# Optimization experiments

Measured on AMD Instinct MI355X. Metric: run time of the kernel, lower is better.

The kernel has to match this reference:

```python
import jax, jax.numpy as jnp
import numpy as np

BSZ, T, L, D = 8, 8, 196, 192
E = D            # expand=1 -> d_inner
C = E * T        # d_inner_s = d_inner * d_t (scan channels)
N = 16           # d_state
K = 4            # d_conv
R = 96           # dt_rank = ceil(d_model*d_t/16)
DT_MIN, DT_MAX, DT_FLOOR = 1e-3, 1e-1, 1e-4


def setup_inputs() -> dict:
    key = jax.random.key(0)
    ks = jax.random.split(key, 9)
    hidden = jax.random.normal(ks[0], (BSZ, T, L, D), jnp.float32)
    in_proj_w = jax.random.normal(ks[1], (2 * E, D), jnp.float32) * (D ** -0.5)
    conv_w = jax.random.normal(ks[2], (C, K), jnp.float32) * 0.2
    conv_b = jax.random.normal(ks[3], (C,), jnp.float32) * 0.05
    x_proj_w = jax.random.normal(ks[4], (R + 2 * N, C), jnp.float32) * (C ** -0.5)
    dt_init_std = R ** -0.5
    dt_proj_w = jax.random.uniform(ks[5], (C, R), jnp.float32, -dt_init_std, dt_init_std)
    dt = jnp.exp(jax.random.uniform(ks[6], (C,), jnp.float32) * (np.log(DT_MAX) - np.log(DT_MIN)) + np.log(DT_MIN))
    dt = jnp.clip(dt, DT_FLOOR)
    dt_bias = dt + jnp.log(-jnp.expm1(-dt))  # inverse-softplus init
    A_log = jnp.log(jnp.tile(jnp.arange(1, N + 1, dtype=jnp.float32), (C, 1)))
    D_param = jnp.ones((C,), jnp.float32)
    return {"hidden": hidden, "in_proj_w": in_proj_w, "conv_w": conv_w, "conv_b": conv_b,
            "x_proj_w": x_proj_w, "dt_proj_w": dt_proj_w, "dt_bias": dt_bias,
            "A_log": A_log, "D_param": D_param}


def _silu(x):
    return x * jax.nn.sigmoid(x)


def reference(hidden, in_proj_w, conv_w, conv_b, x_proj_w, dt_proj_w, dt_bias, A_log, D_param):
    Bsz, T_, L_, D_ = hidden.shape
    E_ = in_proj_w.shape[0] // 2
    # in_proj (no bias): (B,T,L,D) @ (2E,D)^T -> (B,2E,T,L)
    xz = jnp.einsum('btld,ed->betl', hidden, in_proj_w)
    # rearrange 'b d t l -> b (d t) l' then chunk(2, dim=1)
    x = xz[:, :E_].reshape(Bsz, E_ * T_, L_)   # (B, C, L)
    z = xz[:, E_:].reshape(Bsz, E_ * T_, L_)
    # causal depthwise conv1d + silu
    x = jax.lax.conv_general_dilated(
        x, conv_w[:, None, :], window_strides=(1,), padding=[(K - 1, 0)],
        dimension_numbers=('NCH', 'OIH', 'NCH'), feature_group_count=conv_w.shape[0])
    x = _silu(x + conv_b[None, :, None])
    # x_proj -> dt, B, C
    x_dbl = jnp.einsum('bcl,rc->brl', x, x_proj_w)  # (B, R+2N, L)
    dt = x_dbl[:, :R]
    B_ssm = x_dbl[:, R:R + N]        # (B, N, L)
    C_ssm = x_dbl[:, R + N:]         # (B, N, L)
    delta = jax.nn.softplus(jnp.einsum('brl,cr->bcl', dt, dt_proj_w) + dt_bias[None, :, None])
    A = -jnp.exp(A_log)              # (C, N)
    # selective scan: h_l = exp(delta*A) * h_{l-1} + delta*B*x
    dA = jnp.exp(jnp.einsum('bcl,cn->lbcn', delta, A))       # (L,B,C,N)
    dBu = jnp.einsum('bcl,bnl,bcl->lbcn', delta, B_ssm, x)   # (L,B,C,N)

    def step(h, ab):
        a, b = ab
        h = h * a + b
        return h, h

    h0 = jnp.zeros((Bsz, dA.shape[2], dA.shape[3]), x.dtype)
    _, hs = jax.lax.scan(step, h0, (dA, dBu))                # (L,B,C,N)
    y = jnp.einsum('lbcn,bnl->bcl', hs, C_ssm)
    y = y + x * D_param[None, :, None]
    out = y * _silu(z)               # (B, C, L) — fused path output before out_proj
    return out
```

## Files before the change

### kernel.cpp

```cpp
#include <hip/hip_runtime.h>
#include <hip/hip_bf16.h>
#include <cstddef>

#define BSZ 8
#define T_  8
#define L_  196
#define D_  192
#define E_  192
#define C_  1536
#define N_  16
#define K_  4
#define R_  96

typedef __attribute__((ext_vector_type(8))) short short8;
typedef __attribute__((ext_vector_type(4))) float f32x4;
typedef unsigned short ushort_t;

__global__ __launch_bounds__(256) void k_cast_bf16(
    const float* __restrict__ in, ushort_t* __restrict__ out, int n8) {
  int i = blockIdx.x * 256 + threadIdx.x;
  if (i >= n8) return;
  const float4* ip = (const float4*)in;
  float4 v0 = ip[(size_t)i * 2];
  float4 v1 = ip[(size_t)i * 2 + 1];
  union { ushort_t u[8]; uint4 v; } r;
  float f[8] = {v0.x, v0.y, v0.z, v0.w, v1.x, v1.y, v1.z, v1.w};
#pragma unroll
  for (int k = 0; k < 8; k++) {
    unsigned int bits = __float_as_uint(f[k]);
    bits += 0x7FFFu + ((bits >> 16) & 1u);
    r.u[k] = (ushort_t)(bits >> 16);
  }
  ((uint4*)out)[i] = r.v;
}

__global__ __launch_bounds__(256) void k_inproj_mfma(
    const ushort_t* __restrict__ hb, const ushort_t* __restrict__ wb,
    float* __restrict__ xb, float* __restrict__ zb) {
  __shared__ float smem[64][97];
  int tid = threadIdx.x;
  int wave = tid >> 6, lane = tid & 63;
  int m0b = blockIdx.x * 64;
  int n0 = blockIdx.y * 96;
  int row = lane & 15, kg = lane >> 4;
  int m0w = m0b + wave * 16;

  f32x4 acc[6] = {};
  const ushort_t* ap = hb + (size_t)(m0w + row) * 192 + kg * 8;
#pragma unroll
  for (int ks = 0; ks < 6; ks++) {
    short8 a = *(const short8*)(ap + ks * 32);
#pragma unroll
    for (int nt = 0; nt < 6; nt++) {
      short8 b = *(const short8*)(wb + (size_t)(n0 + nt * 16 + row) * 192 + ks * 32 + kg * 8);
      acc[nt] = __builtin_amdgcn_mfma_f32_16x16x32_bf16(a, b, acc[nt], 0, 0, 0);
    }
  }
#pragma unroll
  for (int nt = 0; nt < 6; nt++) {
#pragma unroll
    for (int j = 0; j < 4; j++) {
      smem[wave * 16 + kg * 4 + j][nt * 16 + row] = acc[nt][j];
    }
  }
  __syncthreads();
  int mloc = tid & 63, eof = tid >> 6;
  int m_glob = m0b + mloc;
  int b = m_glob / 1568, u = m_glob % 1568;
  size_t obase = (size_t)b * 301056 + u;
#pragma unroll
  for (int e = eof; e < 96; e += 4) {
    int eg = n0 + e;
    float v = smem[mloc][e];
    if (eg < 192) xb[obase + (size_t)eg * 1568] = v;
    else          zb[obase + (size_t)(eg - 192) * 1568] = v;
  }
}

__global__ __launch_bounds__(256) void k_inproj_f32(
    const float* __restrict__ A, const float* __restrict__ W,
    float* __restrict__ xb, float* __restrict__ zb) {
  __shared__ float As[16][132];
  __shared__ float Bs[16][132];
  int tid = threadIdx.x;
  int m0 = blockIdx.x * 128;
  int n0 = blockIdx.y * 128;
  int tx = tid & 15, ty = tid >> 4;
  float acc[8][8] = {};
  for (int k0 = 0; k0 < 192; k0 += 16) {
#pragma unroll
    for (int i = 0; i < 2; i++) {
      int idx = tid + i * 256;
      int m = idx >> 2, k4 = (idx & 3) * 4;
      float4 v = *(const float4*)&A[(size_t)(m0 + m) * 192 + k0 + k4];
      As[k4 + 0][m] = v.x; As[k4 + 1][m] = v.y;
      As[k4 + 2][m] = v.z; As[k4 + 3][m] = v.w;
    }
#pragma unroll
    for (int i = 0; i < 2; i++) {
      int idx = tid + i * 256;
      int n = idx >> 2, k4 = (idx & 3) * 4;
      float4 v = *(const float4*)&W[(size_t)(n0 + n) * 192 + k0 + k4];
      Bs[k4 + 0][n] = v.x; Bs[k4 + 1][n] = v.y;
      Bs[k4 + 2][n] = v.z; Bs[k4 + 3][n] = v.w;
    }
    __syncthreads();
#pragma unroll
    for (int kk = 0; kk < 16; kk++) {
      float a_[8], b_[8];
      *(float4*)&a_[0] = *(const float4*)&As[kk][ty * 4];
      *(float4*)&a_[4] = *(const float4*)&As[kk][ty * 4 + 64];
      *(float4*)&b_[0] = *(const float4*)&Bs[kk][tx * 4];
      *(float4*)&b_[4] = *(const float4*)&Bs[kk][tx * 4 + 64];
#pragma unroll
      for (int i = 0; i < 8; i++)
#pragma unroll
        for (int j = 0; j < 8; j++) acc[i][j] += a_[i] * b_[j];
    }
    __syncthreads();
  }
#pragma unroll
  for (int i = 0; i < 8; i++) {
    int m = m0 + ty * 4 + (i & 3) + ((i >> 2) * 64);
    int b = m / (T_ * L_);
    int r = m % (T_ * L_);
    int t = r / L_;
    int l = r % L_;
#pragma unroll
    for (int j = 0; j < 8; j++) {
      int e = n0 + tx * 4 + (j & 3) + ((j >> 2) * 64);
      float v = acc[i][j];
      if (e < E_) {
        int c = e * T_ + t;
        xb[((size_t)b * C_ + c) * L_ + l] = v;
      } else {
        int c = (e - E_) * T_ + t;
        zb[((size_t)b * C_ + c) * L_ + l] = v;
      }
    }
  }
}

__global__ __launch_bounds__(256) void k_conv(
    const float* __restrict__ xb, const float* __restrict__ conv_w,
    const float* __restrict__ conv_b, float* __restrict__ xc) {
  int idx = blockIdx.x * 256 + threadIdx.x;
  int l = idx % L_;
  int bc = idx / L_;
  int c = bc % C_;
  const float* xrow = xb + (size_t)bc * L_;
  const float* w = conv_w + c * K_;
  float acc = conv_b[c];
#pragma unroll
  for (int k = 0; k < K_; k++) {
    int ll = l - (K_ - 1) + k;
    if (ll >= 0) acc += xrow[ll] * w[k];
  }
  xc[idx] = acc / (1.f + __expf(-acc));
}

__global__ __launch_bounds__(256) void k_wtrans(
    const float* __restrict__ W, float* __restrict__ Wt) {
  int idx = blockIdx.x * 256 + threadIdx.x;
  int r = idx / 1536;
  int c = idx - r * 1536;
  Wt[(size_t)c * 128 + r] = W[idx];
}

#define XKK 32
__global__ __launch_bounds__(256) void k_xdbl_tile(
    const float* __restrict__ xc, const float* __restrict__ Wt,
    float* __restrict__ part) {
  __shared__ float Ws2[XKK][128];
  __shared__ float Xs[XKK][64];
  int tid = threadIdx.x;
  int n0 = blockIdx.x * 64;
  int c0 = blockIdx.y * 96;
  int tx = tid & 15, ty = tid >> 4;
  float acc[8][4] = {};
  for (int ck = 0; ck < 96; ck += XKK) {
#pragma unroll
    for (int i = 0; i < 4; i++) {
      int idx = tid + i * 256;
      int c = idx >> 5, r4 = (idx & 31) * 4;
      *(float4*)&Ws2[c][r4] = *(const float4*)&Wt[(size_t)(c0 + ck + c) * 128 + r4];
    }
#pragma unroll
    for (int i = 0; i < 8; i++) {
      int idx = tid + i * 256;
      int c = idx >> 6, j = idx & 63;
      int n = n0 + j;
      float v = 0.f;
      if (n < BSZ * L_) {
        int b = n / L_, l = n - b * L_;
        v = xc[((size_t)b * C_ + c0 + ck + c) * L_ + l];
      }
      Xs[c][j] = v;
    }
    __syncthreads();
#pragma unroll
    for (int kk = 0; kk < XKK; kk++) {
      float w_[8], x_[4];
      *(float4*)&w_[0] = *(const float4*)&Ws2[kk][ty * 8];
      *(float4*)&w_[4] = *(const float4*)&Ws2[kk][ty * 8 + 4];
      *(float4*)&x_[0] = *(const float4*)&Xs[kk][tx * 4];
#pragma unroll
      for (int i = 0; i < 8; i++)
#pragma unroll
        for (int j = 0; j < 4; j++) acc[i][j] += w_[i] * x_[j];
    }
    __syncthreads();
  }
  int kc = blockIdx.y;
#pragma unroll
  for (int j = 0; j < 4; j++) {
    int n = n0 + tx * 4 + j;
    if (n < BSZ * L_) {
      int b = n / L_, l = n - b * L_;
      float* pp = &part[(((size_t)kc * 8 + b) * L_ + l) * 128 + ty * 8];
      float4 v0 = {acc[0][j], acc[1][j], acc[2][j], acc[3][j]};
      float4 v1 = {acc[4][j], acc[5][j], acc[6][j], acc[7][j]};
      *(float4*)&pp[0] = v0;
      *(float4*)&pp[4] = v1;
    }
  }
}

__global__ __launch_bounds__(256) void k_xreduce(
    const float* __restrict__ part, float* __restrict__ xdbl,
    float* __restrict__ Bt, float* __restrict__ Ct) {
  int tx = threadIdx.x & 63;
  int ty = threadIdx.x >> 6;
  int l = blockIdx.x * 4 + ty;
  int b = blockIdx.y;
  size_t o = ((size_t)b * L_ + l) * 128 + tx;
  float v0 = 0.f, v1 = 0.f;
#pragma unroll
  for (int kc = 0; kc < 16; kc++) {
    v0 += part[(size_t)kc * (8 * L_ * 128) + o];
    v1 += part[(size_t)kc * (8 * L_ * 128) + o + 64];
  }
  int r1 = tx + 64;
  xdbl[((size_t)b * 96 + tx) * L_ + l] = v0;
  if (r1 < 96) {
    xdbl[((size_t)b * 96 + r1) * L_ + l] = v1;
  } else if (r1 < 96 + N_) {
    Bt[((size_t)b * L_ + l) * N_ + (r1 - 96)] = v1;
  } else {
    Ct[((size_t)b * L_ + l) * N_ + (r1 - 96 - N_)] = v1;
  }
}

__global__ __launch_bounds__(256) void k_xdbl_mono(
    const float* __restrict__ xc, const float* __restrict__ W,
    float* __restrict__ xdbl, float* __restrict__ Bt, float* __restrict__ Ct) {
  int tx = threadIdx.x & 63;
  int ty = threadIdx.x >> 6;
  int l = blockIdx.x * 64 + tx;
  int r0 = blockIdx.y * 4 + ty;
  int r1 = r0 + 64;
  int b = blockIdx.z;
  if (l >= L_) return;
  const float* xcb = xc + (size_t)b * C_ * L_;
  float acc0 = 0.f, acc1 = 0.f;
#pragma unroll 4
  for (int c = 0; c < C_; c++) {
    float v = xcb[(size_t)c * L_ + l];
    acc0 += v * W[(size_t)r0 * C_ + c];
    acc1 += v * W[(size_t)r1 * C_ + c];
  }
  xdbl[((size_t)b * 96 + r0) * L_ + l] = acc0;
  if (r1 < 96) {
    xdbl[((size_t)b * 96 + r1) * L_ + l] = acc1;
  } else if (r1 < 96 + N_) {
    Bt[((size_t)b * L_ + l) * N_ + (r1 - 96)] = acc1;
  } else {
    Ct[((size_t)b * L_ + l) * N_ + (r1 - 96 - N_)] = acc1;
  }
}

__global__ __launch_bounds__(256) void k_delta_gemm(
    const float* __restrict__ dtm, const float* __restrict__ Wdt,
    const float* __restrict__ dt_bias, float* __restrict__ delta) {
  __shared__ float Ws[96][68];
  __shared__ float Ds[96][68];
  int tid = threadIdx.x;
  int n0 = blockIdx.x * 64;
  int c0 = blockIdx.y * 64;
  for (int idx = tid; idx < 64 * 96; idx += 256) {
    int i = idx / 96, r = idx - i * 96;
    Ws[r][i] = Wdt[(size_t)(c0 + i) * 96 + r];
  }
  for (int idx = tid; idx < 96 * 64; idx += 256) {
    int r = idx >> 6, j = idx & 63;
    int n = n0 + j;
    float v = 0.f;
    if (n < BSZ * L_) {
      int b = n / L_, l = n - b * L_;
      v = dtm[((size_t)b * 96 + r) * L_ + l];
    }
    Ds[r][j] = v;
  }
  __syncthreads();
  int tx = tid & 15, ty = tid >> 4;
  float acc[4][4] = {};
#pragma unroll 8
  for (int r = 0; r < 96; r++) {
    float4 av = *(const float4*)&Ws[r][ty * 4];
    float4 bv = *(const float4*)&Ds[r][tx * 4];
    float a_[4] = {av.x, av.y, av.z, av.w};
    float b_[4] = {bv.x, bv.y, bv.z, bv.w};
#pragma unroll
    for (int i = 0; i < 4; i++)
#pragma unroll
      for (int j = 0; j < 4; j++) acc[i][j] += a_[i] * b_[j];
  }
#pragma unroll
  for (int i = 0; i < 4; i++) {
    int c = c0 + ty * 4 + i;
    float bias = dt_bias[c];
#pragma unroll
    for (int j = 0; j < 4; j++) {
      int n = n0 + tx * 4 + j;
      if (n < BSZ * L_) {
        int b = n / L_, l = n - b * L_;
        float v = acc[i][j] + bias;
        float sp = (v > 20.f) ? v : __logf(1.f + __expf(v));
        delta[((size_t)b * C_ + c) * L_ + l] = sp;
      }
    }
  }
}

__global__ __launch_bounds__(512) void k_scan_fused(
    const float* __restrict__ delta, const float* __restrict__ xc,
    const float* __restrict__ zb, const float* __restrict__ Bt,
    const float* __restrict__ Ct, const float* __restrict__ A_log,
    const float* __restrict__ D_param, float* __restrict__ out) {
  __shared__ float BtS[196][20];
  __shared__ float CtS[196][20];
  __shared__ float yS[16][196];
  int tid = threadIdx.x;
  int b = blockIdx.y;
  int c_base = blockIdx.x * 16;
  int wave = tid >> 6, lane = tid & 63;
  int chunk = lane & 15;
  int nl = lane >> 4;
  bool act = chunk < 14;
  const int l0 = chunk * 14;
  int c0 = c_base + wave * 2;
  int c1 = c0 + 1;

  {
    const float4* gB = (const float4*)(Bt + (size_t)b * L_ * N_);
    const float4* gC = (const float4*)(Ct + (size_t)b * L_ * N_);
    for (int i = tid; i < 784; i += 512) {
      int l = i >> 2, q = i & 3;
      *(float4*)&BtS[l][q * 4] = gB[i];
      *(float4*)&CtS[l][q * 4] = gC[i];
    }
  }

  float4 a0, a1;
  {
    float4 t0 = *(const float4*)&A_log[c0 * N_ + nl * 4];
    float4 t1 = *(const float4*)&A_log[c1 * N_ + nl * 4];
    a0.x = -__expf(t0.x); a0.y = -__expf(t0.y);
    a0.z = -__expf(t0.z); a0.w = -__expf(t0.w);
    a1.x = -__expf(t1.x); a1.y = -__expf(t1.y);
    a1.z = -__expf(t1.z); a1.w = -__expf(t1.w);
  }
  size_t w0 = (size_t)(b * C_ + c0) * L_ + l0;
  size_t w1 = (size_t)(b * C_ + c1) * L_ + l0;

  float2 dv0[7], xv0[7], dv1[7], xv1[7];
  if (act) {
    const float2* d2a = (const float2*)(delta + w0);
    const float2* d2b = (const float2*)(delta + w1);
    const float2* x2a = (const float2*)(xc + w0);
    const float2* x2b = (const float2*)(xc + w1);
#pragma unroll
    for (int i = 0; i < 7; i++) {
      dv0[i] = d2a[i]; dv1[i] = d2b[i];
      xv0[i] = x2a[i]; xv1[i] = x2b[i];
    }
  } else {
#pragma unroll
    for (int i = 0; i < 7; i++) {
      dv0[i] = {0.f, 0.f}; dv1[i] = {0.f, 0.f};
      xv0[i] = {0.f, 0.f}; xv1[i] = {0.f, 0.f};
    }
  }
  __syncthreads();

  float4 h0 = {0.f,0.f,0.f,0.f}, p0 = {1.f,1.f,1.f,1.f};
  float4 h1 = {0.f,0.f,0.f,0.f}, p1 = {1.f,1.f,1.f,1.f};
#pragma unroll
  for (int l = 0; l < 14; l++) {
    float d0 = (l & 1) ? dv0[l >> 1].y : dv0[l >> 1].x;
    float d1 = (l & 1) ? dv1[l >> 1].y : dv1[l >> 1].x;
    float x0 = (l & 1) ? xv0[l >> 1].y : xv0[l >> 1].x;
    float x1 = (l & 1) ? xv1[l >> 1].y : xv1[l >> 1].x;
    float du0 = d0 * x0, du1 = d1 * x1;
    float4 Bv = *(const float4*)&BtS[l0 + l][nl * 4];
    float e0x = __expf(d0 * a0.x), e0y = __expf(d0 * a0.y);
    float e0z = __expf(d0 * a0.z), e0w = __expf(d0 * a0.w);
    float e1x = __expf(d1 * a1.x), e1y = __expf(d1 * a1.y);
    float e1z = __expf(d1 * a1.z), e1w = __expf(d1 * a1.w);
    h0.x = h0.x * e0x + du0 * Bv.x; p0.x *= e0x;
    h0.y = h0.y * e0y + du0 * Bv.y; p0.y *= e0y;
    h0.z = h0.z * e0z + du0 * Bv.z; p0.z *= e0z;
    h0.w = h0.w * e0w + du0 * Bv.w; p0.w *= e0w;
    h1.x = h1.x * e1x + du1 * Bv.x; p1.x *= e1x;
    h1.y = h1.y * e1y + du1 * Bv.y; p1.y *= e1y;
    h1.z = h1.z * e1z + du1 * Bv.z; p1.z *= e1z;
    h1.w = h1.w * e1w + du1 * Bv.w; p1.w *= e1w;
  }

#pragma unroll
  for (int s = 1; s < 16; s <<= 1) {
    float4 P0, Q0, P1, Q1;
    P0.x = __shfl_up(p0.x, s, 16); Q0.x = __shfl_up(h0.x, s, 16);
    P0.y = __shfl_up(p0.y, s, 16); Q0.y = __shfl_up(h0.y, s, 16);
    P0.z = __shfl_up(p0.z, s, 16); Q0.z = __shfl_up(h0.z, s, 16);
    P0.w = __shfl_up(p0.w, s, 16); Q0.w = __shfl_up(h0.w, s, 16);
    P1.x = __shfl_up(p1.x, s, 16); Q1.x = __shfl_up(h1.x, s, 16);
    P1.y = __shfl_up(p1.y, s, 16); Q1.y = __shfl_up(h1.y, s, 16);
    P1.z = __shfl_up(p1.z, s, 16); Q1.z = __shfl_up(h1.z, s, 16);
    P1.w = __shfl_up(p1.w, s, 16); Q1.w = __shfl_up(h1.w, s, 16);
    if (chunk >= s) {
      h0.x = p0.x * Q0.x + h0.x; p0.x *= P0.x;
      h0.y = p0.y * Q0.y + h0.y; p0.y *= P0.y;
      h0.z = p0.z * Q0.z + h0.z; p0.z *= P0.z;
      h0.w = p0.w * Q0.w + h0.w; p0.w *= P0.w;
      h1.x = p1.x * Q1.x + h1.x; p1.x *= P1.x;
      h1.y = p1.y * Q1.y + h1.y; p1.y *= P1.y;
      h1.z = p1.z * Q1.z + h1.z; p1.z *= P1.z;
      h1.w = p1.w * Q1.w + h1.w; p1.w *= P1.w;
    }
  }
  float4 g0, g1;
  g0.x = __shfl_up(h0.x, 1, 16); g1.x = __shfl_up(h1.x, 1, 16);
  g0.y = __shfl_up(h0.y, 1, 16); g1.y = __shfl_up(h1.y, 1, 16);
  g0.z = __shfl_up(h0.z, 1, 16); g1.z = __shfl_up(h1.z, 1, 16);
  g0.w = __shfl_up(h0.w, 1, 16); g1.w = __shfl_up(h1.w, 1, 16);
  if (chunk == 0) {
    g0.x = g0.y = g0.z = g0.w = 0.f;
    g1.x = g1.y = g1.z = g1.w = 0.f;
  }

  if (act) {
#pragma unroll
    for (int l = 0; l < 14; l++) {
      float d0 = (l & 1) ? dv0[l >> 1].y : dv0[l >> 1].x;
      float d1 = (l & 1) ? dv1[l >> 1].y : dv1[l >> 1].x;
      float x0 = (l & 1) ? xv0[l >> 1].y : xv0[l >> 1].x;
      float x1 = (l & 1) ? xv1[l >> 1].y : xv1[l >> 1].x;
      float du0 = d0 * x0, du1 = d1 * x1;
      float4 Bv = *(const float4*)&BtS[l0 + l][nl * 4];
      float4 Cv = *(const float4*)&CtS[l0 + l][nl * 4];
      float e0x = __expf(d0 * a0.x), e0y = __expf(d0 * a0.y);
      float e0z = __expf(d0 * a0.z), e0w = __expf(d0 * a0.w);
      float e1x = __expf(d1 * a1.x), e1y = __expf(d1 * a1.y);
      float e1z = __expf(d1 * a1.z), e1w = __expf(d1 * a1.w);
      g0.x = g0.x * e0x + du0 * Bv.x;
      g0.y = g0.y * e0y + du0 * Bv.y;
      g0.z = g0.z * e0z + du0 * Bv.z;
      g0.w = g0.w * e0w + du0 * Bv.w;
      g1.x = g1.x * e1x + du1 * Bv.x;
      g1.y = g1.y * e1y + du1 * Bv.y;
      g1.z = g1.z * e1z + du1 * Bv.z;
      g1.w = g1.w * e1w + du1 * Bv.w;
      float y0 = g0.x * Cv.x + g0.y * Cv.y + g0.z * Cv.z + g0.w * Cv.w;
      float y1 = g1.x * Cv.x + g1.y * Cv.y + g1.z * Cv.z + g1.w * Cv.w;
      y0 += __shfl_xor(y0, 16);
      y0 += __shfl_xor(y0, 32);
      y1 += __shfl_xor(y1, 16);
      y1 += __shfl_xor(y1, 32);
      if (nl == 0) {
        yS[wave * 2 + 0][l0 + l] = y0;
        yS[wave * 2 + 1][l0 + l] = y1;
      }
    }
  }
  __syncthreads();

  size_t base = (size_t)(b * C_ + c_base) * L_;
  for (int idx = tid; idx < 16 * L_; idx += 512) {
    int cloc = idx / L_, l = idx - cloc * L_;
    float y = yS[cloc][l];
    float xv = xc[base + idx];
    float zv = zb[base + idx];
    float Dp = D_param[c_base + cloc];
    float sz = zv / (1.f + __expf(-zv));
    out[base + idx] = (y + xv * Dp) * sz;
  }
}

extern "C" void kernel_launch(void* const* d_in, const int* in_sizes, int n_in,
                              void* d_out, int out_size, void* d_ws, size_t ws_size,
                              hipStream_t stream) {
  const float* hidden    = (const float*)d_in[0];
  const float* in_proj_w = (const float*)d_in[1];
  const float* conv_w    = (const float*)d_in[2];
  const float* conv_b    = (const float*)d_in[3];
  const float* x_proj_w  = (const float*)d_in[4];
  const float* dt_proj_w = (const float*)d_in[5];
  const float* dt_bias   = (const float*)d_in[6];
  const float* A_log     = (const float*)d_in[7];
  const float* D_param   = (const float*)d_in[8];
  float* out = (float*)d_out;

  const size_t NBCL  = (size_t)BSZ * C_ * L_;
  const size_t NDT   = (size_t)BSZ * 96 * L_;
  const size_t NBT   = (size_t)BSZ * L_ * N_;
  const size_t NPART = (size_t)16 * BSZ * L_ * 128;
  const size_t NWT   = (size_t)C_ * 128;
  const size_t NHID  = (size_t)BSZ * T_ * L_ * D_;
  const size_t NW1   = (size_t)2 * E_ * D_;
  float* ws = (float*)d_ws;
  float* xb    = ws;
  float* zb    = xb + NBCL;
  float* xc    = zb + NBCL;
  float* xdbl  = xc + NBCL;
  float* BtArr = xdbl + NDT;
  float* CtArr = BtArr + NBT;
  float* Pbuf  = CtArr + NBT;
  float* delta = xb;

  size_t base_floats = 3 * NBCL + NDT + 2 * NBT;
  size_t avail = ws_size / 4 > base_floats ? ws_size / 4 - base_floats : 0;
  bool split_ok = avail >= NPART + NWT;

  if (split_ok) {
    ushort_t* hb = (ushort_t*)Pbuf;
    ushort_t* wb = hb + NHID;
    k_cast_bf16<<<(int)((NHID / 8 + 255) / 256), 256, 0, stream>>>(hidden, hb, (int)(NHID / 8));
    k_cast_bf16<<<(int)((NW1 / 8 + 255) / 256), 256, 0, stream>>>(in_proj_w, wb, (int)(NW1 / 8));
    k_inproj_mfma<<<dim3(196, 4), 256, 0, stream>>>(hb, wb, xb, zb);
  } else {
    k_inproj_f32<<<dim3(98, 3), 256, 0, stream>>>(hidden, in_proj_w, xb, zb);
  }

  k_conv<<<(int)(NBCL / 256), 256, 0, stream>>>(xb, conv_w, conv_b, xc);

  if (split_ok) {
    float* part = Pbuf;
    float* Wt   = Pbuf + NPART;
    k_wtrans<<<(int)(NWT / 256), 256, 0, stream>>>(x_proj_w, Wt);
    k_xdbl_tile<<<dim3(25, 16), 256, 0, stream>>>(xc, Wt, part);
    k_xreduce<<<dim3(49, BSZ), 256, 0, stream>>>(part, xdbl, BtArr, CtArr);
  } else {
    k_xdbl_mono<<<dim3(4, 16, BSZ), 256, 0, stream>>>(xc, x_proj_w, xdbl, BtArr, CtArr);
  }

  k_delta_gemm<<<dim3(25, 24), 256, 0, stream>>>(xdbl, dt_proj_w, dt_bias, delta);

  k_scan_fused<<<dim3(C_ / 16, BSZ), 512, 0, stream>>>(delta, xc, zb, BtArr, CtArr,
                                                       A_log, D_param, out);
}
```

Before: 125.2 us.

## Fuse causal conv+SiLU into x_proj and scan, merge casts, drop transpose kernel

The standalone depthwise conv+SiLU kernel is removed. Its output is now recomputed on the fly from the in_proj output inside the x_proj tile GEMM and inside the fused scan kernel. This saves a full write and re-read of the conv activation buffer and one launch. The two bf16 cast kernels are merged into a single launch. The x_proj weight transpose kernel is replaced by transposing into padded shared memory during the tile load. In exchange, conv arithmetic and overlapping neighbour loads are repeated in two consumers, and register pressure in the scan kernel rises.

```diff
diff --git a/kernel.cpp b/kernel.cpp
--- a/kernel.cpp
+++ b/kernel.cpp
@@ -16,13 +16,18 @@
 typedef __attribute__((ext_vector_type(4))) float f32x4;
 typedef unsigned short ushort_t;
 
-__global__ __launch_bounds__(256) void k_cast_bf16(
-    const float* __restrict__ in, ushort_t* __restrict__ out, int n8) {
+__global__ __launch_bounds__(256) void k_cast_all(
+    const float* __restrict__ hidden, const float* __restrict__ w,
+    ushort_t* __restrict__ hb, ushort_t* __restrict__ wb) {
+  const int H8 = 301056;
+  const int T8 = H8 + 9216;
   int i = blockIdx.x * 256 + threadIdx.x;
-  if (i >= n8) return;
-  const float4* ip = (const float4*)in;
-  float4 v0 = ip[(size_t)i * 2];
-  float4 v1 = ip[(size_t)i * 2 + 1];
+  if (i >= T8) return;
+  const float4* ip; uint4* op; int j;
+  if (i < H8) { ip = (const float4*)hidden; op = (uint4*)hb; j = i; }
+  else        { ip = (const float4*)w;      op = (uint4*)wb; j = i - H8; }
+  float4 v0 = ip[(size_t)j * 2];
+  float4 v1 = ip[(size_t)j * 2 + 1];
   union { ushort_t u[8]; uint4 v; } r;
   float f[8] = {v0.x, v0.y, v0.z, v0.w, v1.x, v1.y, v1.z, v1.w};
 #pragma unroll
@@ -31,7 +36,7 @@
     bits += 0x7FFFu + ((bits >> 16) & 1u);
     r.u[k] = (ushort_t)(bits >> 16);
   }
-  ((uint4*)out)[i] = r.v;
+  op[j] = r.v;
 }
 
 __global__ __launch_bounds__(256) void k_inproj_mfma(
@@ -159,19 +164,12 @@
   xc[idx] = acc / (1.f + __expf(-acc));
 }
 
-__global__ __launch_bounds__(256) void k_wtrans(
-    const float* __restrict__ W, float* __restrict__ Wt) {
-  int idx = blockIdx.x * 256 + threadIdx.x;
-  int r = idx / 1536;
-  int c = idx - r * 1536;
-  Wt[(size_t)c * 128 + r] = W[idx];
-}
-
 #define XKK 32
 __global__ __launch_bounds__(256) void k_xdbl_tile(
-    const float* __restrict__ xc, const float* __restrict__ Wt,
+    const float* __restrict__ xb, const float* __restrict__ conv_w,
+    const float* __restrict__ conv_b, const float* __restrict__ W,
     float* __restrict__ part) {
-  __shared__ float Ws2[XKK][128];
+  __shared__ float Ws2[XKK][132];
   __shared__ float Xs[XKK][64];
   int tid = threadIdx.x;
   int n0 = blockIdx.x * 64;
@@ -180,20 +178,31 @@
   float acc[8][4] = {};
   for (int ck = 0; ck < 96; ck += XKK) {
 #pragma unroll
-    for (int i = 0; i < 4; i++) {
-      int idx = tid + i * 256;
-      int c = idx >> 5, r4 = (idx & 31) * 4;
-      *(float4*)&Ws2[c][r4] = *(const float4*)&Wt[(size_t)(c0 + ck + c) * 128 + r4];
-    }
-#pragma unroll
-    for (int i = 0; i < 8; i++) {
-      int idx = tid + i * 256;
+    for (int p = 0; p < 4; p++) {
+      int idx = tid + p * 256;
+      int r = idx >> 3;
+      int c4 = (idx & 7) * 4;
+      float4 w4 = *(const float4*)&W[(size_t)r * 1536 + c0 + ck + c4];
+      Ws2[c4 + 0][r] = w4.x; Ws2[c4 + 1][r] = w4.y;
+      Ws2[c4 + 2][r] = w4.z; Ws2[c4 + 3][r] = w4.w;
+    }
+#pragma unroll
+    for (int p = 0; p < 8; p++) {
+      int idx = tid + p * 256;
       int c = idx >> 6, j = idx & 63;
       int n = n0 + j;
       float v = 0.f;
       if (n < BSZ * L_) {
         int b = n / L_, l = n - b * L_;
-        v = xc[((size_t)b * C_ + c0 + ck + c) * L_ + l];
+        int cc = c0 + ck + c;
+        const float* row = xb + ((size_t)b * C_ + cc) * L_;
+        float s = conv_b[cc];
+#pragma unroll
+        for (int k = 0; k < K_; k++) {
+          int ll = l - 3 + k;
+          if (ll >= 0) s += row[ll] * conv_w[cc * K_ + k];
+        }
+        v = s / (1.f + __expf(-s));
       }
       Xs[c][j] = v;
     }
@@ -333,7 +342,8 @@
 }
 
 __global__ __launch_bounds__(512) void k_scan_fused(
-    const float* __restrict__ delta, const float* __restrict__ xc,
+    const float* __restrict__ delta, const float* __restrict__ xb,
+    const float* __restrict__ conv_w, const float* __restrict__ conv_b,
     const float* __restrict__ zb, const float* __restrict__ Bt,
     const float* __restrict__ Ct, const float* __restrict__ A_log,
     const float* __restrict__ D_param, float* __restrict__ out) {
@@ -373,23 +383,41 @@
   size_t w0 = (size_t)(b * C_ + c0) * L_ + l0;
   size_t w1 = (size_t)(b * C_ + c1) * L_ + l0;
 
-  float2 dv0[7], xv0[7], dv1[7], xv1[7];
+  float xr0[14], xr1[14];
+  {
+    const float* r0 = xb + (size_t)(b * C_ + c0) * L_;
+    const float* r1 = xb + (size_t)(b * C_ + c1) * L_;
+    float t0[17], t1[17];
+#pragma unroll
+    for (int i = 0; i < 17; i++) {
+      int ll = l0 - 3 + i;
+      bool ok = act && ll >= 0;
+      t0[i] = ok ? r0[ll] : 0.f;
+      t1[i] = ok ? r1[ll] : 0.f;
+    }
+    float w00 = conv_w[c0 * K_ + 0], w01 = conv_w[c0 * K_ + 1];
+    float w02 = conv_w[c0 * K_ + 2], w03 = conv_w[c0 * K_ + 3];
+    float w10 = conv_w[c1 * K_ + 0], w11 = conv_w[c1 * K_ + 1];
+    float w12 = conv_w[c1 * K_ + 2], w13 = conv_w[c1 * K_ + 3];
+    float cb0 = conv_b[c0], cb1 = conv_b[c1];
+#pragma unroll
+    for (int l = 0; l < 14; l++) {
+      float s0 = cb0 + t0[l] * w00 + t0[l + 1] * w01 + t0[l + 2] * w02 + t0[l + 3] * w03;
+      float s1 = cb1 + t1[l] * w10 + t1[l + 1] * w11 + t1[l + 2] * w12 + t1[l + 3] * w13;
+      xr0[l] = s0 / (1.f + __expf(-s0));
+      xr1[l] = s1 / (1.f + __expf(-s1));
+    }
+  }
+
+  float2 dv0[7], dv1[7];
   if (act) {
     const float2* d2a = (const float2*)(delta + w0);
     const float2* d2b = (const float2*)(delta + w1);
-    const float2* x2a = (const float2*)(xc + w0);
-    const float2* x2b = (const float2*)(xc + w1);
-#pragma unroll
-    for (int i = 0; i < 7; i++) {
-      dv0[i] = d2a[i]; dv1[i] = d2b[i];
-      xv0[i] = x2a[i]; xv1[i] = x2b[i];
-    }
+#pragma unroll
+    for (int i = 0; i < 7; i++) { dv0[i] = d2a[i]; dv1[i] = d2b[i]; }
   } else {
 #pragma unroll
-    for (int i = 0; i < 7; i++) {
-      dv0[i] = {0.f, 0.f}; dv1[i] = {0.f, 0.f};
-      xv0[i] = {0.f, 0.f}; xv1[i] = {0.f, 0.f};
-    }
+    for (int i = 0; i < 7; i++) { dv0[i] = {0.f, 0.f}; dv1[i] = {0.f, 0.f}; }
   }
   __syncthreads();
 
@@ -399,9 +427,7 @@
   for (int l = 0; l < 14; l++) {
     float d0 = (l & 1) ? dv0[l >> 1].y : dv0[l >> 1].x;
     float d1 = (l & 1) ? dv1[l >> 1].y : dv1[l >> 1].x;
-    float x0 = (l & 1) ? xv0[l >> 1].y : xv0[l >> 1].x;
-    float x1 = (l & 1) ? xv1[l >> 1].y : xv1[l >> 1].x;
-    float du0 = d0 * x0, du1 = d1 * x1;
+    float du0 = d0 * xr0[l], du1 = d1 * xr1[l];
     float4 Bv = *(const float4*)&BtS[l0 + l][nl * 4];
     float e0x = __expf(d0 * a0.x), e0y = __expf(d0 * a0.y);
     float e0z = __expf(d0 * a0.z), e0w = __expf(d0 * a0.w);
@@ -454,9 +480,7 @@
     for (int l = 0; l < 14; l++) {
       float d0 = (l & 1) ? dv0[l >> 1].y : dv0[l >> 1].x;
       float d1 = (l & 1) ? dv1[l >> 1].y : dv1[l >> 1].x;
-      float x0 = (l & 1) ? xv0[l >> 1].y : xv0[l >> 1].x;
-      float x1 = (l & 1) ? xv1[l >> 1].y : xv1[l >> 1].x;
-      float du0 = d0 * x0, du1 = d1 * x1;
+      float du0 = d0 * xr0[l], du1 = d1 * xr1[l];
       float4 Bv = *(const float4*)&BtS[l0 + l][nl * 4];
       float4 Cv = *(const float4*)&CtS[l0 + l][nl * 4];
       float e0x = __expf(d0 * a0.x), e0y = __expf(d0 * a0.y);
@@ -488,10 +512,18 @@
   size_t base = (size_t)(b * C_ + c_base) * L_;
   for (int idx = tid; idx < 16 * L_; idx += 512) {
     int cloc = idx / L_, l = idx - cloc * L_;
+    int c = c_base + cloc;
+    const float* xrow = xb + base + (size_t)cloc * L_;
+    float s = conv_b[c];
+#pragma unroll
+    for (int k = 0; k < K_; k++) {
+      int ll = l - 3 + k;
+      if (ll >= 0) s += xrow[ll] * conv_w[c * K_ + k];
+    }
+    float xv = s / (1.f + __expf(-s));
     float y = yS[cloc][l];
-    float xv = xc[base + idx];
     float zv = zb[base + idx];
-    float Dp = D_param[c_base + cloc];
+    float Dp = D_param[c];
     float sz = zv / (1.f + __expf(-zv));
     out[base + idx] = (y + xv * Dp) * sz;
   }
@@ -515,47 +547,38 @@
   const size_t NDT   = (size_t)BSZ * 96 * L_;
   const size_t NBT   = (size_t)BSZ * L_ * N_;
   const size_t NPART = (size_t)16 * BSZ * L_ * 128;
-  const size_t NWT   = (size_t)C_ * 128;
   const size_t NHID  = (size_t)BSZ * T_ * L_ * D_;
-  const size_t NW1   = (size_t)2 * E_ * D_;
   float* ws = (float*)d_ws;
   float* xb    = ws;
   float* zb    = xb + NBCL;
-  float* xc    = zb + NBCL;
-  float* xdbl  = xc + NBCL;
+  float* slot3 = zb + NBCL;
+  float* xdbl  = slot3 + NBCL;
   float* BtArr = xdbl + NDT;
   float* CtArr = BtArr + NBT;
   float* Pbuf  = CtArr + NBT;
-  float* delta = xb;
+  float* delta = slot3;
 
   size_t base_floats = 3 * NBCL + NDT + 2 * NBT;
   size_t avail = ws_size / 4 > base_floats ? ws_size / 4 - base_floats : 0;
-  bool split_ok = avail >= NPART + NWT;
+  bool split_ok = avail >= NPART;
 
   if (split_ok) {
     ushort_t* hb = (ushort_t*)Pbuf;
     ushort_t* wb = hb + NHID;
-    k_cast_bf16<<<(int)((NHID / 8 + 255) / 256), 256, 0, stream>>>(hidden, hb, (int)(NHID / 8));
-    k_cast_bf16<<<(int)((NW1 / 8 + 255) / 256), 256, 0, stream>>>(in_proj_w, wb, (int)(NW1 / 8));
+    k_cast_all<<<1212, 256, 0, stream>>>(hidden, in_proj_w, hb, wb);
     k_inproj_mfma<<<dim3(196, 4), 256, 0, stream>>>(hb, wb, xb, zb);
+    float* part = Pbuf;
+    k_xdbl_tile<<<dim3(25, 16), 256, 0, stream>>>(xb, conv_w, conv_b, x_proj_w, part);
+    k_xreduce<<<dim3(49, BSZ), 256, 0, stream>>>(part, xdbl, BtArr, CtArr);
   } else {
     k_inproj_f32<<<dim3(98, 3), 256, 0, stream>>>(hidden, in_proj_w, xb, zb);
-  }
-
-  k_conv<<<(int)(NBCL / 256), 256, 0, stream>>>(xb, conv_w, conv_b, xc);
-
-  if (split_ok) {
-    float* part = Pbuf;
-    float* Wt   = Pbuf + NPART;
-    k_wtrans<<<(int)(NWT / 256), 256, 0, stream>>>(x_proj_w, Wt);
-    k_xdbl_tile<<<dim3(25, 16), 256, 0, stream>>>(xc, Wt, part);
-    k_xreduce<<<dim3(49, BSZ), 256, 0, stream>>>(part, xdbl, BtArr, CtArr);
-  } else {
-    k_xdbl_mono<<<dim3(4, 16, BSZ), 256, 0, stream>>>(xc, x_proj_w, xdbl, BtArr, CtArr);
+    k_conv<<<(int)(NBCL / 256), 256, 0, stream>>>(xb, conv_w, conv_b, slot3);
+    k_xdbl_mono<<<dim3(4, 16, BSZ), 256, 0, stream>>>(slot3, x_proj_w, xdbl, BtArr, CtArr);
   }
 
   k_delta_gemm<<<dim3(25, 24), 256, 0, stream>>>(xdbl, dt_proj_w, dt_bias, delta);
 
-  k_scan_fused<<<dim3(C_ / 16, BSZ), 512, 0, stream>>>(delta, xc, zb, BtArr, CtArr,
+  k_scan_fused<<<dim3(C_ / 16, BSZ), 512, 0, stream>>>(delta, xb, conv_w, conv_b,
+                                                       zb, BtArr, CtArr,
                                                        A_log, D_param, out);
 }
```

After: 148.5 us. +18.6%, slower.
